# Optimization experiments

Measured on AMD Instinct MI355X. Metric: run time of the kernel, lower is better.

The kernel has to match this reference:

```python
import jax, jax.numpy as jnp
import numpy as np

H = 16  # num_heads


def setup_inputs() -> dict:
    key = jax.random.key(0)
    ks = jax.random.split(key, 9)
    L, N, E, I = 2048, 2, 2048, 2048
    s = 0.02
    return {
        "query": jax.random.normal(ks[0], (L, N, E), jnp.float32),
        "q_proj": jax.random.normal(ks[1], (I, E), jnp.float32) * s,
        "q_bias": jax.random.normal(ks[2], (I,), jnp.float32) * s,
        "k_proj": jax.random.normal(ks[3], (I, E), jnp.float32) * s,
        "k_bias": jax.random.normal(ks[4], (I,), jnp.float32) * s,
        "v_proj": jax.random.normal(ks[5], (I, E), jnp.float32) * s,
        "v_bias": jax.random.normal(ks[6], (I,), jnp.float32) * s,
        "out_proj": jax.random.normal(ks[7], (E, I), jnp.float32) * s,
        "out_bias": jax.random.normal(ks[8], (E,), jnp.float32) * s,
    }


def reference(query, q_proj, q_bias, k_proj, k_bias, v_proj, v_bias, out_proj, out_bias):
    L, N, E = query.shape
    h = H
    d = q_proj.shape[0] // h
    scale = d ** (-0.5)

    def split_heads(x):
        # [L, N, h*d] -> [N, h, L, d]  (matches view(L, N*h, d).transpose(0,1))
        return x.reshape(L, N, h, d).transpose(1, 2, 0, 3)

    q = split_heads(query @ q_proj.T + q_bias) * scale
    k = split_heads(query @ k_proj.T + k_bias)
    v = split_heads(query @ v_proj.T + v_bias)

    scores = jnp.einsum('nhld,nhkd->nhlk', q, k)  # [N, h, L, L]
    causal = jnp.tril(jnp.ones((L, L), dtype=bool))
    scores = jnp.where(causal, scores, jnp.float32(-10000.0))
    attn = jax.nn.softmax(scores, axis=-1)
    # dropout_p = 0.0 -> identity
    ctx = jnp.einsum('nhlk,nhkd->nhld', attn, v)
    ctx = ctx.transpose(2, 0, 1, 3).reshape(L, N, h * d)  # [L, N, h*d]
    return ctx @ out_proj.T + out_bias  # [L, N, E]
```

## Files before the change

### kernel.cpp

```cpp
#include <hip/hip_runtime.h>
#include <stdint.h>

#define L_SEQ 2048
#define NB 2
#define EMB 2048
#define II 2048
#define NH 16
#define DH 128
#define MROWS (L_SEQ * NB)

typedef __attribute__((ext_vector_type(8))) short bf16x8;
typedef __attribute__((ext_vector_type(4))) float f32x4;
typedef unsigned short u16;
typedef unsigned int u32;

__device__ __forceinline__ u16 f2bf(float f) {
  u32 u = __builtin_bit_cast(u32, f);
  u = u + 0x7fffu + ((u >> 16) & 1u);
  return (u16)(u >> 16);
}
__device__ __forceinline__ u16 f2bf_trunc(float f) {
  return (u16)(__builtin_bit_cast(u32, f) >> 16);
}

__device__ __forceinline__ void gl_lds16(const void* g, const u16* l) {
  __builtin_amdgcn_global_load_lds(
      (const __attribute__((address_space(1))) void*)(uintptr_t)g,
      (__attribute__((address_space(3))) void*)(u32)(uintptr_t)l, 16, 0, 0);
}

__global__ __launch_bounds__(256) void cast_all(
    const float* __restrict__ q, const float* __restrict__ w0, const float* __restrict__ w1,
    const float* __restrict__ w2, const float* __restrict__ w3, u16* __restrict__ dq,
    u16* __restrict__ dw) {
  const int b = blockIdx.x, t = threadIdx.x;
  const float* src;
  u16* dst;
  int idx;
  if (b < 8192) {
    src = q; dst = dq; idx = b * 256 + t;
  } else {
    int u = b - 8192;
    int sel = u >> 12;
    src = (sel == 0) ? w0 : (sel == 1) ? w1 : (sel == 2) ? w2 : w3;
    dst = dw + (size_t)sel * II * EMB;
    idx = (u & 4095) * 256 + t;
  }
  float4 v = ((const float4*)src)[idx];
  ushort4 o;
  o.x = f2bf(v.x); o.y = f2bf(v.y); o.z = f2bf(v.z); o.w = f2bf(v.w);
  ((ushort4*)dst)[idx] = o;
}

__global__ __launch_bounds__(256) void transpose_v(const u16* __restrict__ V,
                                                   u16* __restrict__ Vt) {
  __shared__ u16 tile[128][72];
  const int lb = blockIdx.x * 64;
  const int h = blockIdx.y;
  const u16* src = V + (size_t)h * L_SEQ * DH;
  u16* dst = Vt + (size_t)h * DH * L_SEQ;
  const int t = threadIdx.x;
  {
    const int l = t & 63, d0 = (t >> 6) * 32;
#pragma unroll
    for (int c = 0; c < 4; c++) {
      uint4 u = *(const uint4*)(src + (size_t)(lb + l) * DH + d0 + c * 8);
      const u16* e = (const u16*)&u;
#pragma unroll
      for (int x = 0; x < 8; x++) tile[d0 + c * 8 + x][l] = e[x];
    }
  }
  __syncthreads();
  {
    const int d = t >> 1, lc = (t & 1) * 32;
#pragma unroll
    for (int c = 0; c < 4; c++) {
      uint4 u = *(const uint4*)&tile[d][lc + c * 8];
      *(uint4*)(dst + (size_t)d * L_SEQ + lb + lc + c * 8) = u;
    }
  }
}

#define BK8 64
#define NT8 (EMB / BK8)

__global__ __launch_bounds__(512, 2) void gemm_qkv_8p(
    const u16* __restrict__ A, const u16* __restrict__ B, const float* __restrict__ qb,
    const float* __restrict__ kb, const float* __restrict__ vb, u16* __restrict__ out_bf,
    float qscale) {
  __shared__ __align__(16) u16 sm[2][32768];
  const int t = threadIdx.x;
  const int lane = t & 63, wv = t >> 6;
  const int quad = lane >> 4, l15 = lane & 15, x7 = l15 & 7;
  const int wm2 = wv >> 2, wn4 = wv & 3;
  const int srow = lane >> 3;
  const int schunk = (lane & 7) ^ (lane >> 3);

  const int bid = blockIdx.x;
  const int swz = (bid & 7) * 48 + (bid >> 3);
  const int bxx = swz >> 4;
  const int byy = swz & 15;
  const int n0 = bxx * 256, m0 = byy * 256;

  const u16* abase = A + (size_t)m0 * EMB;
  const u16* bbase = B + (size_t)n0 * EMB;

  auto stageA = [&](u16* buf, int k0, int u) {
    int row = u * 64 + wv * 8 + srow;
    gl_lds16(abase + (size_t)row * EMB + k0 + schunk * 8, buf + u * 4096 + wv * 512);
  };
  auto stageB = [&](u16* buf, int k0, int u) {
    int row = u * 64 + wv * 8 + srow;
    gl_lds16(bbase + (size_t)row * EMB + k0 + schunk * 8, buf + 16384 + u * 4096 + wv * 512);
  };

  stageB(sm[0], 0, 0); stageB(sm[0], 0, 1); stageB(sm[0], 0, 2); stageB(sm[0], 0, 3);
  stageA(sm[0], 0, 0); stageA(sm[0], 0, 2); stageA(sm[0], 0, 1); stageA(sm[0], 0, 3);
  __asm__ volatile("s_waitcnt vmcnt(2)" ::: "memory");
  __builtin_amdgcn_s_barrier();

  f32x4 acc[8][4] = {};
  bf16x8 afr[4][2];

#pragma unroll 1
  for (int tt = 0; tt < NT8; ++tt) {
    const u16* cur = sm[tt & 1];
    u16* nxt = sm[(tt + 1) & 1];
    const int kn = (tt + 1) * BK8;
    const bool pf = (tt + 1 < NT8);

    {
#pragma unroll
      for (int mi = 0; mi < 4; mi++)
#pragma unroll
        for (int ks = 0; ks < 2; ks++)
          afr[mi][ks] =
              *(const bf16x8*)(cur + (wm2 * 128 + mi * 16 + l15) * 64 + (((ks * 4 + quad) ^ x7)) * 8);
      bf16x8 bfr2[2][2];
#pragma unroll
      for (int nj = 0; nj < 2; nj++)
#pragma unroll
        for (int ks = 0; ks < 2; ks++)
          bfr2[nj][ks] = *(const bf16x8*)(cur + 16384 + (wn4 * 64 + nj * 16 + l15) * 64 +
                                          (((ks * 4 + quad) ^ x7)) * 8);
      if (pf) { stageB(nxt, kn, 0); stageB(nxt, kn, 1); }
      __builtin_amdgcn_s_barrier();
      __builtin_amdgcn_s_setprio(1);
#pragma unroll
      for (int ks = 0; ks < 2; ks++)
#pragma unroll
        for (int mi = 0; mi < 4; mi++)
#pragma unroll
          for (int nj = 0; nj < 2; nj++)
            acc[mi][nj] =
                __builtin_amdgcn_mfma_f32_16x16x32_bf16(afr[mi][ks], bfr2[nj][ks], acc[mi][nj], 0, 0, 0);
      __builtin_amdgcn_s_setprio(0);
      __builtin_amdgcn_s_barrier();
    }

    {
      bf16x8 bfr2[2][2];
#pragma unroll
      for (int nj = 0; nj < 2; nj++)
#pragma unroll
        for (int ks = 0; ks < 2; ks++)
          bfr2[nj][ks] = *(const bf16x8*)(cur + 16384 + (wn4 * 64 + (nj + 2) * 16 + l15) * 64 +
                                          (((ks * 4 + quad) ^ x7)) * 8);
      if (pf) {
        stageB(nxt, kn, 2); stageB(nxt, kn, 3);
        __asm__ volatile("s_waitcnt vmcnt(4)" ::: "memory");
      } else {
        __asm__ volatile("s_waitcnt vmcnt(0)" ::: "memory");
      }
      __builtin_amdgcn_s_barrier();
      __builtin_amdgcn_s_setprio(1);
#pragma unroll
      for (int ks = 0; ks < 2; ks++)
#pragma unroll
        for (int mi = 0; mi < 4; mi++)
#pragma unroll
          for (int nj = 0; nj < 2; nj++)
            acc[mi][nj + 2] =
                __builtin_amdgcn_mfma_f32_16x16x32_bf16(afr[mi][ks], bfr2[nj][ks], acc[mi][nj + 2], 0, 0, 0);
      __builtin_amdgcn_s_setprio(0);
      __builtin_amdgcn_s_barrier();
    }

    {
#pragma unroll
      for (int mi = 0; mi < 4; mi++)
#pragma unroll
        for (int ks = 0; ks < 2; ks++)
          afr[mi][ks] = *(const bf16x8*)(cur + (wm2 * 128 + (mi + 4) * 16 + l15) * 64 +
                                         (((ks * 4 + quad) ^ x7)) * 8);
      bf16x8 bfr2[2][2];
#pragma unroll
      for (int nj = 0; nj < 2; nj++)
#pragma unroll
        for (int ks = 0; ks < 2; ks++)
          bfr2[nj][ks] = *(const bf16x8*)(cur + 16384 + (wn4 * 64 + nj * 16 + l15) * 64 +
                                          (((ks * 4 + quad) ^ x7)) * 8);
      if (pf) { stageA(nxt, kn, 0); stageA(nxt, kn, 2); }
      __builtin_amdgcn_s_barrier();
      __builtin_amdgcn_s_setprio(1);
#pragma unroll
      for (int ks = 0; ks < 2; ks++)
#pragma unroll
        for (int mi = 0; mi < 4; mi++)
#pragma unroll
          for (int nj = 0; nj < 2; nj++)
            acc[mi + 4][nj] =
                __builtin_amdgcn_mfma_f32_16x16x32_bf16(afr[mi][ks], bfr2[nj][ks], acc[mi + 4][nj], 0, 0, 0);
      __builtin_amdgcn_s_setprio(0);
      __builtin_amdgcn_s_barrier();
    }

    {
      bf16x8 bfr2[2][2];
#pragma unroll
      for (int nj = 0; nj < 2; nj++)
#pragma unroll
        for (int ks = 0; ks < 2; ks++)
          bfr2[nj][ks] = *(const bf16x8*)(cur + 16384 + (wn4 * 64 + (nj + 2) * 16 + l15) * 64 +
                                          (((ks * 4 + quad) ^ x7)) * 8);
      if (pf) {
        stageA(nxt, kn, 1); stageA(nxt, kn, 3);
        __asm__ volatile("s_waitcnt vmcnt(2)" ::: "memory");
      }
      __builtin_amdgcn_s_barrier();
      __builtin_amdgcn_s_setprio(1);
#pragma unroll
      for (int ks = 0; ks < 2; ks++)
#pragma unroll
        for (int mi = 0; mi < 4; mi++)
#pragma unroll
          for (int nj = 0; nj < 2; nj++)
            acc[mi + 4][nj + 2] =
                __builtin_amdgcn_mfma_f32_16x16x32_bf16(afr[mi][ks], bfr2[nj][ks], acc[mi + 4][nj + 2], 0, 0, 0);
      __builtin_amdgcn_s_setprio(0);
      __builtin_amdgcn_s_barrier();
    }
  }

  const int mat = n0 >> 11;
  const float* bp = (mat == 0) ? qb : (mat == 1) ? kb : vb;
  const float sc2 = (mat == 0) ? qscale : 1.0f;
#pragma unroll
  for (int mi = 0; mi < 8; mi++) {
#pragma unroll
    for (int nj = 0; nj < 4; nj++) {
#pragma unroll
      for (int r = 0; r < 4; r++) {
        int row = m0 + wm2 * 128 + mi * 16 + quad * 4 + r;
        int col = n0 + wn4 * 64 + nj * 16 + l15;
        int cc = col & 2047;
        float v = (acc[mi][nj][r] + bp[cc]) * sc2;
        int l = row >> 1, nb = row & 1;
        int hh = cc >> 7, dd = cc & 127;
        out_bf[(size_t)mat * MROWS * II + ((size_t)(nb * NH + hh) * L_SEQ + l) * DH + dd] =
            f2bf(v);
      }
    }
  }
}

__global__ __launch_bounds__(256) void gemm_nt(
    const u16* __restrict__ A, const u16* __restrict__ B, const float* __restrict__ b0,
    const float* __restrict__ b1, const float* __restrict__ b2, u16* __restrict__ out_bf,
    float* __restrict__ out_f, int Nd, int K, float qscale, int mode) {
  __shared__ __align__(16) u16 a_sm[128 * 64];
  __shared__ __align__(16) u16 b_sm[128 * 64];
  const int t = threadIdx.x;
  const int lane = t & 63, wv = t >> 6;
  const int quad = lane >> 4, l15 = lane & 15;
  const int x7 = l15 & 7;
  const int wm = (wv >> 1) * 64, wn = (wv & 1) * 64;
  const int m0 = blockIdx.y * 128, n0 = blockIdx.x * 128;
  const int srow = lane >> 3;
  const int schunk = (lane & 7) ^ (lane >> 3);

  f32x4 acc[4][4] = {};
  const u16* abase = A + (size_t)m0 * K;
  const u16* bbase = B + (size_t)n0 * K;

  for (int k0 = 0; k0 < K; k0 += 64) {
    __syncthreads();
#pragma unroll
    for (int j = 0; j < 4; j++) {
      int ci = wv * 4 + j;
      int row = ci * 8 + srow;
      gl_lds16(abase + (size_t)row * K + k0 + schunk * 8, a_sm + ci * 512);
      gl_lds16(bbase + (size_t)row * K + k0 + schunk * 8, b_sm + ci * 512);
    }
    __syncthreads();
#pragma unroll
    for (int ks = 0; ks < 2; ks++) {
      bf16x8 af[4], bfr[4];
#pragma unroll
      for (int i = 0; i < 4; i++)
        af[i] = *(const bf16x8*)(a_sm + (wm + i * 16 + l15) * 64 + ((ks * 4 + quad) ^ x7) * 8);
#pragma unroll
      for (int j = 0; j < 4; j++)
        bfr[j] = *(const bf16x8*)(b_sm + (wn + j * 16 + l15) * 64 + ((ks * 4 + quad) ^ x7) * 8);
#pragma unroll
      for (int i = 0; i < 4; i++)
#pragma unroll
        for (int j = 0; j < 4; j++)
          acc[i][j] = __builtin_amdgcn_mfma_f32_16x16x32_bf16(af[i], bfr[j], acc[i][j], 0, 0, 0);
    }
  }

  const int mat = n0 >> 11;
  const float* bp = (mode == 1) ? b0 : (mat == 0 ? b0 : (mat == 1 ? b1 : b2));
  const float sc2 = (mode == 0 && mat == 0) ? qscale : 1.0f;
#pragma unroll
  for (int i = 0; i < 4; i++) {
#pragma unroll
    for (int j = 0; j < 4; j++) {
#pragma unroll
      for (int r = 0; r < 4; r++) {
        int row = m0 + wm + i * 16 + quad * 4 + r;
        int col = n0 + wn + j * 16 + l15;
        if (mode == 0) {
          int cc = col & 2047;
          float v = (acc[i][j][r] + bp[cc]) * sc2;
          int l = row >> 1, nb = row & 1;
          int hh = cc >> 7, dd = cc & 127;
          out_bf[(size_t)mat * MROWS * II + ((size_t)(nb * NH + hh) * L_SEQ + l) * DH + dd] =
              f2bf(v);
        } else {
          out_f[(size_t)row * Nd + col] = acc[i][j][r] + bp[col];
        }
      }
    }
  }
}

__global__ __launch_bounds__(256, 2) void flash_attn(
    const u16* __restrict__ Qh, const u16* __restrict__ Kh, const u16* __restrict__ Vt,
    u16* __restrict__ ctx) {
  __shared__ __align__(16) u16 k_sm[128 * 128];
  __shared__ __align__(16) u16 v_sm[128 * 128];
  const int bx = blockIdx.x;
  const int nh = ((bx & 7) << 2) | ((bx >> 3) & 3);
  const int g = (bx >> 5) & 7;
  const int qt = (bx < 256) ? (15 - g) : g;
  const int q0 = qt * 128;
  const int nK = qt + 1;
  const int t = threadIdx.x;
  const int lane = t & 63, wv = t >> 6;
  const int quad = lane >> 4, l15 = lane & 15;
  const int x7 = l15 & 7;
  const size_t hq = (size_t)nh * L_SEQ * DH;
  const u16* qp = Qh + hq;
  const u16* kp = Kh + hq;
  const u16* vp = Vt + hq;
  const int n = nh >> 4, h = nh & 15;
  const int srow = lane >> 4;
  const int spos = lane & 15;
  u16* pw = k_sm + wv * 4096;

  bf16x8 qf[2][4];
#pragma unroll
  for (int mi = 0; mi < 2; mi++)
#pragma unroll
    for (int ks = 0; ks < 4; ks++)
      qf[mi][ks] = *(const bf16x8*)(qp + (size_t)(q0 + wv * 32 + mi * 16 + l15) * DH +
                                    ks * 32 + quad * 8);

  f32x4 o_acc[2][8] = {};
  float l_part[2][4] = {};

#pragma unroll 1
  for (int jb = 0; jb < nK; jb++) {
    const int kb = jb * 128;
    __syncthreads();
#pragma unroll
    for (int i = 0; i < 8; i++) {
      int ci = wv * 8 + i;
      int row = ci * 4 + srow;
      int gc = spos ^ (row & 7);
      gl_lds16(kp + (size_t)(kb + row) * DH + gc * 8, k_sm + ci * 512);
      gl_lds16(vp + (size_t)row * L_SEQ + kb + gc * 8, v_sm + ci * 512);
    }
    __syncthreads();

    f32x4 s[2][8] = {};
    __builtin_amdgcn_s_setprio(1);
#pragma unroll
    for (int nt = 0; nt < 8; nt++) {
#pragma unroll
      for (int ks = 0; ks < 4; ks++) {
        bf16x8 kf = *(const bf16x8*)(k_sm + (nt * 16 + l15) * 128 + ((ks * 4 + quad) ^ x7) * 8);
#pragma unroll
        for (int mi = 0; mi < 2; mi++)
          s[mi][nt] = __builtin_amdgcn_mfma_f32_16x16x32_bf16(qf[mi][ks], kf, s[mi][nt], 0, 0, 0);
      }
    }
    __builtin_amdgcn_s_setprio(0);
    __syncthreads();

    const bool diag = (jb == qt);
#pragma unroll
    for (int mi = 0; mi < 2; mi++) {
      const int rowg = q0 + wv * 32 + mi * 16 + quad * 4;
#pragma unroll
      for (int nt = 0; nt < 8; nt++) {
        const int colg = kb + nt * 16 + l15;
#pragma unroll
        for (int r = 0; r < 4; r++) {
          float p = __builtin_amdgcn_exp2f(s[mi][nt][r]);
          if (diag && colg > rowg + r) p = 0.f;
          l_part[mi][r] += p;
          int pr = mi * 16 + quad * 4 + r;
          int chunk = nt * 2 + (l15 >> 3);
          int pos = chunk ^ (pr & 7);
          pw[pr * 128 + pos * 8 + (l15 & 7)] = f2bf_trunc(p);
        }
      }
    }
    __asm__ volatile("s_waitcnt lgkmcnt(0)" ::: "memory");

    bf16x8 pf[2][4];
#pragma unroll
    for (int mi = 0; mi < 2; mi++)
#pragma unroll
      for (int ks = 0; ks < 4; ks++)
        pf[mi][ks] = *(const bf16x8*)(pw + (mi * 16 + l15) * 128 + ((ks * 4 + quad) ^ x7) * 8);
    __builtin_amdgcn_s_setprio(1);
#pragma unroll
    for (int nt = 0; nt < 8; nt++) {
#pragma unroll
      for (int ks = 0; ks < 4; ks++) {
        bf16x8 vf = *(const bf16x8*)(v_sm + (nt * 16 + l15) * 128 + ((ks * 4 + quad) ^ x7) * 8);
#pragma unroll
        for (int mi = 0; mi < 2; mi++)
          o_acc[mi][nt] =
              __builtin_amdgcn_mfma_f32_16x16x32_bf16(pf[mi][ks], vf, o_acc[mi][nt], 0, 0, 0);
      }
    }
    __builtin_amdgcn_s_setprio(0);
  }

#pragma unroll
  for (int mi = 0; mi < 2; mi++) {
#pragma unroll
    for (int r = 0; r < 4; r++) {
      float lv = l_part[mi][r];
#pragma unroll
      for (int off = 1; off < 16; off <<= 1) lv += __shfl_xor(lv, off, 64);
      float inv = 1.f / lv;
      const int lrow = q0 + wv * 32 + mi * 16 + quad * 4 + r;
#pragma unroll
      for (int nt = 0; nt < 8; nt++) {
        int dd = nt * 16 + l15;
        ctx[((size_t)lrow * NB + n) * EMB + h * DH + dd] = f2bf(o_acc[mi][nt][r] * inv);
      }
    }
  }
}

extern "C" void kernel_launch(void* const* d_in, const int* in_sizes, int n_in,
                              void* d_out, int out_size, void* d_ws, size_t ws_size,
                              hipStream_t stream) {
  const float* query    = (const float*)d_in[0];
  const float* q_proj   = (const float*)d_in[1];
  const float* q_bias   = (const float*)d_in[2];
  const float* k_proj   = (const float*)d_in[3];
  const float* k_bias   = (const float*)d_in[4];
  const float* v_proj   = (const float*)d_in[5];
  const float* v_bias   = (const float*)d_in[6];
  const float* out_proj = (const float*)d_in[7];
  const float* out_bias = (const float*)d_in[8];

  u16* ws  = (u16*)d_ws;
  u16* Xbf = ws;
  u16* Wq  = Xbf + (size_t)MROWS * EMB;
  u16* Wk  = Wq + (size_t)II * EMB;
  u16* Wv  = Wk + (size_t)II * EMB;
  u16* Wo  = Wv + (size_t)II * EMB;
  u16* Qw  = Wo + (size_t)EMB * II;
  u16* Kw  = Qw + (size_t)MROWS * II;
  u16* Vw  = Kw + (size_t)MROWS * II;
  u16* Cw  = Vw + (size_t)MROWS * II;
  u16* Vtb = Xbf;

  cast_all<<<8192 + 4 * 4096, 256, 0, stream>>>(query, q_proj, k_proj, v_proj, out_proj,
                                                Xbf, Wq);

  const float qscale = 0.08838834764831845f * 1.4426950408889634f;
  gemm_qkv_8p<<<384, 512, 0, stream>>>(Xbf, Wq, q_bias, k_bias, v_bias, Qw, qscale);

  transpose_v<<<dim3(L_SEQ / 64, NB * NH), 256, 0, stream>>>(Vw, Vtb);

  flash_attn<<<512, 256, 0, stream>>>(Qw, Kw, Vtb, Cw);

  gemm_nt<<<dim3(EMB / 128, MROWS / 128), 256, 0, stream>>>(
      Cw, Wo, out_bias, nullptr, nullptr, nullptr, (float*)d_out, EMB, II, 1.0f, 1);
}
```

Baseline: 442.1 us.

## Prefetch A tile halves two k-steps ahead in QKV GEMM pipeline

Restructures the global-to-LDS staging schedule of the projection GEMM so that half of the A tile for step t+2 is issued into the current buffer after its rows are consumed. All of B for t+1 is now issued in the first quarter, and the vmcnt wait counts are adjusted to match. The aim is deeper memory latency hiding with the same two LDS buffers. It risks races, because the early A writes overwrite rows of the current buffer that other waves may still be reading, and the changed waitcnt accounting is fragile.

Measured after the change: 447.0 us. No clear change (+1.1%).

```diff
diff --git a/kernel.cpp b/kernel.cpp
--- a/kernel.cpp
+++ b/kernel.cpp
@@ -105,18 +105,22 @@
   const u16* abase = A + (size_t)m0 * EMB;
   const u16* bbase = B + (size_t)n0 * EMB;
 
-  auto stageA = [&](u16* buf, int k0, int u) {
+  auto stageA = [&](int buf, int k0, int u) {
     int row = u * 64 + wv * 8 + srow;
-    gl_lds16(abase + (size_t)row * EMB + k0 + schunk * 8, buf + u * 4096 + wv * 512);
+    const u16* dst = (buf ? sm[1] : sm[0]) + u * 4096 + wv * 512;
+    gl_lds16(abase + (size_t)row * EMB + k0 + schunk * 8, dst);
   };
-  auto stageB = [&](u16* buf, int k0, int u) {
+  auto stageB = [&](int buf, int k0, int u) {
     int row = u * 64 + wv * 8 + srow;
-    gl_lds16(bbase + (size_t)row * EMB + k0 + schunk * 8, buf + 16384 + u * 4096 + wv * 512);
+    const u16* dst = (buf ? sm[1] : sm[0]) + 16384 + u * 4096 + wv * 512;
+    gl_lds16(bbase + (size_t)row * EMB + k0 + schunk * 8, dst);
   };
 
-  stageB(sm[0], 0, 0); stageB(sm[0], 0, 1); stageB(sm[0], 0, 2); stageB(sm[0], 0, 3);
-  stageA(sm[0], 0, 0); stageA(sm[0], 0, 2); stageA(sm[0], 0, 1); stageA(sm[0], 0, 3);
-  __asm__ volatile("s_waitcnt vmcnt(2)" ::: "memory");
+  stageA(0, 0, 0); stageA(0, 0, 2);
+  stageB(0, 0, 0); stageB(0, 0, 1); stageB(0, 0, 2); stageB(0, 0, 3);
+  stageA(0, 0, 1); stageA(0, 0, 3);
+  stageA(1, BK8, 0); stageA(1, BK8, 2);
+  __asm__ volatile("s_waitcnt vmcnt(4)" ::: "memory");
   __builtin_amdgcn_s_barrier();
 
   f32x4 acc[8][4] = {};
@@ -124,10 +128,12 @@
 
 #pragma unroll 1
   for (int tt = 0; tt < NT8; ++tt) {
-    const u16* cur = sm[tt & 1];
-    u16* nxt = sm[(tt + 1) & 1];
-    const int kn = (tt + 1) * BK8;
-    const bool pf = (tt + 1 < NT8);
+    const int cb = tt & 1, nb_ = (tt + 1) & 1;
+    const u16* cur = cb ? sm[1] : sm[0];
+    const int kn1 = (tt + 1) * BK8;
+    const int kn2 = (tt + 2) * BK8;
+    const bool pf1 = (tt + 1 < NT8);
+    const bool pf2 = (tt + 2 < NT8);
 
     {
 #pragma unroll
@@ -143,7 +149,7 @@
         for (int ks = 0; ks < 2; ks++)
           bfr2[nj][ks] = *(const bf16x8*)(cur + 16384 + (wn4 * 64 + nj * 16 + l15) * 64 +
                                           (((ks * 4 + quad) ^ x7)) * 8);
-      if (pf) { stageB(nxt, kn, 0); stageB(nxt, kn, 1); }
+      if (pf1) { stageB(nb_, kn1, 0); stageB(nb_, kn1, 1); stageB(nb_, kn1, 2); stageB(nb_, kn1, 3); }
       __builtin_amdgcn_s_barrier();
       __builtin_amdgcn_s_setprio(1);
 #pragma unroll
@@ -166,9 +172,9 @@
         for (int ks = 0; ks < 2; ks++)
           bfr2[nj][ks] = *(const bf16x8*)(cur + 16384 + (wn4 * 64 + (nj + 2) * 16 + l15) * 64 +
                                           (((ks * 4 + quad) ^ x7)) * 8);
-      if (pf) {
-        stageB(nxt, kn, 2); stageB(nxt, kn, 3);
-        __asm__ volatile("s_waitcnt vmcnt(4)" ::: "memory");
+      if (pf1) {
+        stageA(nb_, kn1, 1); stageA(nb_, kn1, 3);
+        __asm__ volatile("s_waitcnt vmcnt(8)" ::: "memory");
       } else {
         __asm__ volatile("s_waitcnt vmcnt(0)" ::: "memory");
       }
@@ -200,7 +206,7 @@
         for (int ks = 0; ks < 2; ks++)
           bfr2[nj][ks] = *(const bf16x8*)(cur + 16384 + (wn4 * 64 + nj * 16 + l15) * 64 +
                                           (((ks * 4 + quad) ^ x7)) * 8);
-      if (pf) { stageA(nxt, kn, 0); stageA(nxt, kn, 2); }
+      if (pf2) { stageA(cb, kn2, 0); stageA(cb, kn2, 2); }
       __builtin_amdgcn_s_barrier();
       __builtin_amdgcn_s_setprio(1);
 #pragma unroll
@@ -223,8 +229,9 @@
         for (int ks = 0; ks < 2; ks++)
           bfr2[nj][ks] = *(const bf16x8*)(cur + 16384 + (wn4 * 64 + (nj + 2) * 16 + l15) * 64 +
                                           (((ks * 4 + quad) ^ x7)) * 8);
-      if (pf) {
-        stageA(nxt, kn, 1); stageA(nxt, kn, 3);
+      if (pf2) {
+        __asm__ volatile("s_waitcnt vmcnt(4)" ::: "memory");
+      } else if (pf1) {
         __asm__ volatile("s_waitcnt vmcnt(2)" ::: "memory");
       }
       __builtin_amdgcn_s_barrier();
```
